# Performance work log

Measured on AMD Instinct MI355X. Metric: run time of the kernel, lower is better.

Reference implementation:

```python
import jax, jax.numpy as jnp
import numpy as np

C_M = 256   # norm_channel (msa channel)
C_Z = 128   # pair_channel
H = 8       # num_head
C = 32      # attention_channel per head


def layer_norm(x, gamma, beta, eps=1e-5):
    mu = jnp.mean(x, axis=-1, keepdims=True)
    var = jnp.var(x, axis=-1, keepdims=True)
    return (x - mu) * jax.lax.rsqrt(var + eps) * gamma + beta


def setup_inputs() -> dict:
    key = jax.random.key(0)
    ks = jax.random.split(key, 12)
    B, S, R = 1, 128, 256
    inp = {
        "msa_act": jax.random.normal(ks[0], (B, S, R, C_M), jnp.float32),
        "pair_act": jax.random.normal(ks[1], (B, R, R, C_Z), jnp.float32),
        "msa_mask": jnp.ones((B, S, R), jnp.float32),
        # query_norm params
        "qn_g": jnp.ones((C_M,), jnp.float32),
        "qn_b": jnp.zeros((C_M,), jnp.float32),
        # feat_2d_norm params
        "pn_g": jnp.ones((C_Z,), jnp.float32),
        "pn_b": jnp.zeros((C_Z,), jnp.float32),
        # feat_2d_weights: Linear(C_Z -> H, bias=False)
        "w2d": jax.random.normal(ks[2], (C_Z, H), jnp.float32) / np.sqrt(C_Z),
        # attention projections [C_M, H, C]
        "wq": jax.random.normal(ks[3], (C_M, H, C), jnp.float32) / np.sqrt(C_M),
        "wk": jax.random.normal(ks[4], (C_M, H, C), jnp.float32) / np.sqrt(C_M),
        "wv": jax.random.normal(ks[5], (C_M, H, C), jnp.float32) / np.sqrt(C_M),
        # gating linear [C_M, H, C] + bias
        "wg": jax.random.normal(ks[6], (C_M, H, C), jnp.float32) / np.sqrt(C_M),
        "bg": jnp.ones((H, C), jnp.float32),
        # output linear [H, C, C_M] + bias
        "wo": jax.random.normal(ks[7], (H, C, C_M), jnp.float32) / np.sqrt(H * C),
        "bo": jnp.zeros((C_M,), jnp.float32),
    }
    return inp


def reference(msa_act, pair_act, msa_mask, qn_g, qn_b, pn_g, pn_b, w2d,
              wq, wk, wv, wg, bg, wo, bo):
    # Pair bias: LayerNorm -> Linear(C_Z->H) -> permute to [B, 1, H, R, R]
    z = layer_norm(pair_act, pn_g, pn_b)            # [B, R, R, C_Z]
    z = jnp.einsum('bqkc,ch->bhqk', z, w2d)          # [B, H, R, R]
    z = z[:, None]                                   # [B, 1, H, R, R]

    # Mask bias: [B, S, 1, 1, R]
    mask_bias = (1e9 * (msa_mask - 1.0))[:, :, None, None, :]

    # Row-wise MHA with query norm
    m = layer_norm(msa_act, qn_g, qn_b)              # [B, S, R, C_M]
    scale = 1.0 / np.sqrt(C)
    q = jnp.einsum('bsqc,chd->bshqd', m, wq) * scale
    k = jnp.einsum('bskc,chd->bshkd', m, wk)
    v = jnp.einsum('bskc,chd->bshkd', m, wv)

    logits = jnp.einsum('bshqd,bshkd->bshqk', q, k) + mask_bias + z
    a = jax.nn.softmax(logits, axis=-1)              # [B, S, H, R, R]
    o = jnp.einsum('bshqk,bshkd->bsqhd', a, v)       # [B, S, R, H, C]

    g = jax.nn.sigmoid(jnp.einsum('bsqc,chd->bsqhd', m, wg) + bg)
    o = o * g
    out = jnp.einsum('bsqhd,hdc->bsqc', o, wo) + bo  # [B, S, R, C_M]
    return out
```

## Files before the change

### kernel.cpp

```cpp
#include <hip/hip_runtime.h>
#include <hip/hip_bf16.h>

typedef unsigned short u16;
typedef __attribute__((ext_vector_type(8))) short bf16x8;
typedef __attribute__((ext_vector_type(4))) float f32x4;

__device__ __forceinline__ float bf2f(u16 u){
  union { unsigned int i; float f; } v; v.i = ((unsigned int)u) << 16; return v.f;
}
__device__ __forceinline__ u16 f2bf(float f){
  union { float f; unsigned int i; } v; v.f = f;
  unsigned int i = v.i;
  return (u16)((i + 0x7fffu + ((i >> 16) & 1u)) >> 16);
}
__device__ __forceinline__ unsigned int pk2(float a, float b){
  union { __hip_bfloat162 v; unsigned int u; } c;
  c.v = __float22bfloat162_rn(float2{a, b});
  return c.u;
}
__device__ __forceinline__ float ldin(const void* p, int i, int f){
  return f ? ((const float*)p)[i] : bf2f(((const u16*)p)[i]);
}

__global__ __launch_bounds__(256) void k_prep(
    const void* __restrict__ msa,  const void* __restrict__ pair,
    const void* __restrict__ qng,  const void* __restrict__ qnb,
    const void* __restrict__ png,  const void* __restrict__ pnb,
    const void* __restrict__ w2d,
    const void* __restrict__ wq, const void* __restrict__ wk,
    const void* __restrict__ wv, const void* __restrict__ wg,
    const void* __restrict__ wo,
    u16* __restrict__ Wt, u16* __restrict__ wot,
    u16* __restrict__ m_bf, u16* __restrict__ z_bf,
    int* __restrict__ flagp)
{
  __shared__ u16 shm[11008];
  __shared__ int flag_sh;
  const int t = threadIdx.x;
  const int bid = blockIdx.x;

  if (t < 64) {
    const unsigned int* msa_w = (const unsigned int*)msa;
    int lo0 = 0, expok = 0;
    #pragma unroll
    for (int j = 0; j < 4; ++j) {
      unsigned int w = msa_w[t * 4 + j];
      if ((w & 0xffffu) == 0u) lo0++;
      unsigned int e = (w >> 7) & 0xffu;
      if (e >= 110u && e <= 140u) expok++;
    }
    #pragma unroll
    for (int off = 1; off < 64; off <<= 1) {
      lo0   += __shfl_xor(lo0,   off, 64);
      expok += __shfl_xor(expok, off, 64);
    }
    if (t == 0) flag_sh = (lo0 > 200) ? 1 : ((expok > 200) ? 0 : 1);
  }
  __syncthreads();
  const int flag = flag_sh;
  if (bid == 0 && t == 0) *flagp = flag;

  if (bid < 80) {
    u16* T = shm;
    const int mat = bid >> 4, tile = bid & 15;
    const int R0 = (tile >> 2) * 64, C0 = (tile & 3) * 64;
    const void* src = (mat == 0) ? wq : (mat == 1) ? wk : (mat == 2) ? wv
                    : (mat == 3) ? wg : wo;
    u16* dst = (mat < 4) ? (Wt + mat * 65536) : wot;
    {
      int i = t >> 2, j0 = (t & 3) * 16;
      #pragma unroll
      for (int e = 0; e < 8; ++e) {
        float a = ldin(src, (R0 + i) * 256 + C0 + j0 + 2*e,     flag);
        float b = ldin(src, (R0 + i) * 256 + C0 + j0 + 2*e + 1, flag);
        *(unsigned int*)(T + i * 72 + j0 + 2*e) = pk2(a, b);
      }
    }
    __syncthreads();
    {
      int j = t >> 2, i0 = (t & 3) * 16;
      u16 o[16];
      #pragma unroll
      for (int e = 0; e < 16; ++e) o[e] = T[(i0 + e) * 72 + j];
      *(uint4*)(dst + (C0 + j) * 256 + R0 + i0)     = *(const uint4*)o;
      *(uint4*)(dst + (C0 + j) * 256 + R0 + i0 + 8) = *(const uint4*)(o + 8);
    }
  } else if (bid < 8272) {
    int wave = t >> 6, lane = t & 63;
    int row = (bid - 80) * 4 + wave;
    float x[4];
    if (flag) {
      float4 f4 = *((const float4*)msa + row * 64 + lane);
      x[0]=f4.x; x[1]=f4.y; x[2]=f4.z; x[3]=f4.w;
    } else {
      uint2 u = *((const uint2*)msa + row * 64 + lane);
      const u16* h = (const u16*)&u;
      #pragma unroll
      for (int j = 0; j < 4; ++j) x[j] = bf2f(h[j]);
    }
    float s = 0.f, sq = 0.f;
    #pragma unroll
    for (int j = 0; j < 4; ++j) { s += x[j]; sq += x[j] * x[j]; }
    #pragma unroll
    for (int off = 1; off < 64; off <<= 1) {
      s  += __shfl_xor(s,  off, 64);
      sq += __shfl_xor(sq, off, 64);
    }
    float mu = s * (1.f / 256.f);
    float var = sq * (1.f / 256.f) - mu * mu;
    float rs = rsqrtf(var + 1e-5f);
    float y[4];
    #pragma unroll
    for (int j = 0; j < 4; ++j) {
      int c = lane * 4 + j;
      y[j] = (x[j] - mu) * rs * ldin(qng, c, flag) + ldin(qnb, c, flag);
    }
    uint2 o2;
    o2.x = pk2(y[0], y[1]);
    o2.y = pk2(y[2], y[3]);
    *((uint2*)m_bf + row * 64 + lane) = o2;
  } else {
    u16* As = shm;
    u16* Bs = shm + 64 * 136;
    const int lane = t & 63, wave = t >> 6;
    const int g = lane >> 4, l15 = lane & 15;
    const int rowBase = (bid - 8272) * 64;

    if (t < 128) {
      #pragma unroll
      for (int n = 0; n < 16; ++n)
        Bs[n * 136 + t] = (n < 8) ? f2bf(ldin(w2d, t * 8 + n, flag)) : (u16)0;
    }
    {
      int lrow = t >> 2, cb = (t & 3) * 32;
      int base = (rowBase + lrow) * 128 + cb;
      float x[32];
      if (flag) {
        const float* p = (const float*)pair + base;
        #pragma unroll
        for (int j = 0; j < 8; ++j) {
          float4 f4 = *(const float4*)(p + 4 * j);
          x[4*j] = f4.x; x[4*j+1] = f4.y; x[4*j+2] = f4.z; x[4*j+3] = f4.w;
        }
      } else {
        const u16* p = (const u16*)pair + base;
        #pragma unroll
        for (int j = 0; j < 4; ++j) {
          uint4 u = *(const uint4*)(p + 8 * j);
          const u16* h = (const u16*)&u;
          #pragma unroll
          for (int e = 0; e < 8; ++e) x[8*j+e] = bf2f(h[e]);
        }
      }
      float s = 0.f, sq = 0.f;
      #pragma unroll
      for (int j = 0; j < 32; ++j) { s += x[j]; sq += x[j] * x[j]; }
      s  += __shfl_xor(s, 1, 64);  s  += __shfl_xor(s, 2, 64);
      sq += __shfl_xor(sq, 1, 64); sq += __shfl_xor(sq, 2, 64);
      float mu = s * (1.f / 128.f);
      float var = sq * (1.f / 128.f) - mu * mu;
      float rs = rsqrtf(var + 1e-5f);
      float n_[32];
      #pragma unroll
      for (int j = 0; j < 32; ++j) {
        int c = cb + j;
        n_[j] = (x[j] - mu) * rs * ldin(png, c, flag) + ldin(pnb, c, flag);
      }
      u16* dst = As + lrow * 136 + cb;
      #pragma unroll
      for (int j = 0; j < 16; ++j)
        *(unsigned int*)(dst + 2*j) = pk2(n_[2*j], n_[2*j+1]);
    }
    __syncthreads();

    f32x4 accz = {0.f, 0.f, 0.f, 0.f};
    #pragma unroll
    for (int kb = 0; kb < 4; ++kb) {
      bf16x8 a = *(const bf16x8*)(As + (wave * 16 + l15) * 136 + kb * 32 + g * 8);
      bf16x8 b = *(const bf16x8*)(Bs + l15 * 136 + kb * 32 + g * 8);
      accz = __builtin_amdgcn_mfma_f32_16x16x32_bf16(a, b, accz, 0, 0, 0);
    }
    if (l15 < 8) {
      #pragma unroll
      for (int r = 0; r < 4; ++r)
        z_bf[l15 * 65536 + rowBase + wave * 16 + g * 4 + r] = f2bf(accz[r]);
    }
  }
}

__global__ __launch_bounds__(256, 2) void k_fused(
    const u16* __restrict__ m_bf, const u16* __restrict__ Wt,
    const void* __restrict__ bg, const u16* __restrict__ z_bf,
    const void* __restrict__ mask, const int* __restrict__ flagp,
    u16* __restrict__ og_ws)
{
  __shared__ u16 Ks[256 * 40];
  __shared__ u16 Vts[32 * 264];
  __shared__ float Mb[256];
  const int flag = *flagp;
  const int t = threadIdx.x, lane = t & 63, wave = t >> 6;
  const int s_ = blockIdx.x, h = blockIdx.y;
  const int g = lane >> 4, l15 = lane & 15;

  Mb[t] = 1e9f * (ldin(mask, s_ * 256 + t, flag) - 1.0f);

  const float scale = 0.17677669529663687f;
  f32x4 zero = {0.f, 0.f, 0.f, 0.f};

  bf16x8 af[8][4];
  #pragma unroll
  for (int kb = 0; kb < 8; ++kb)
    #pragma unroll
    for (int mt = 0; mt < 4; ++mt)
      af[kb][mt] = *(const bf16x8*)(
          m_bf + (s_ * 256 + wave * 64 + mt * 16 + l15) * 256 + kb * 32 + g * 8);

  unsigned int qp[4][4];
  float gg[4][2][4];

  #pragma unroll
  for (int matid = 0; matid < 4; ++matid) {
    const u16* W = Wt + matid * 65536 + (h * 32) * 256;
    f32x4 acc[4][2];
    #pragma unroll
    for (int mt = 0; mt < 4; ++mt) { acc[mt][0] = zero; acc[mt][1] = zero; }
    #pragma unroll
    for (int kb = 0; kb < 8; ++kb) {
      bf16x8 b0 = *(const bf16x8*)(W + l15 * 256        + kb * 32 + g * 8);
      bf16x8 b1 = *(const bf16x8*)(W + (16 + l15) * 256 + kb * 32 + g * 8);
      #pragma unroll
      for (int mt = 0; mt < 4; ++mt) {
        if (matid == 0 || matid == 2) {
          acc[mt][0] = __builtin_amdgcn_mfma_f32_16x16x32_bf16(b0, af[kb][mt], acc[mt][0], 0, 0, 0);
          acc[mt][1] = __builtin_amdgcn_mfma_f32_16x16x32_bf16(b1, af[kb][mt], acc[mt][1], 0, 0, 0);
        } else {
          acc[mt][0] = __builtin_amdgcn_mfma_f32_16x16x32_bf16(af[kb][mt], b0, acc[mt][0], 0, 0, 0);
          acc[mt][1] = __builtin_amdgcn_mfma_f32_16x16x32_bf16(af[kb][mt], b1, acc[mt][1], 0, 0, 0);
        }
      }
    }
    if (matid == 0) {
      #pragma unroll
      for (int mt = 0; mt < 4; ++mt) {
        qp[mt][0] = pk2(acc[mt][0][0] * scale, acc[mt][0][1] * scale);
        qp[mt][1] = pk2(acc[mt][0][2] * scale, acc[mt][0][3] * scale);
        qp[mt][2] = pk2(acc[mt][1][0] * scale, acc[mt][1][1] * scale);
        qp[mt][3] = pk2(acc[mt][1][2] * scale, acc[mt][1][3] * scale);
      }
    } else if (matid == 1) {
      #pragma unroll
      for (int mt = 0; mt < 4; ++mt)
        #pragma unroll
        for (int r = 0; r < 4; ++r) {
          int rowl = wave * 64 + mt * 16 + g * 4 + r;
          Ks[rowl * 40 + l15]      = f2bf(acc[mt][0][r]);
          Ks[rowl * 40 + 16 + l15] = f2bf(acc[mt][1][r]);
        }
    } else if (matid == 2) {
      #pragma unroll
      for (int mt = 0; mt < 4; ++mt)
        #pragma unroll
        for (int r = 0; r < 4; ++r) {
          int kcol = wave * 64 + mt * 16 + l15;
          Vts[(g * 4 + r) * 264 + kcol]      = f2bf(acc[mt][0][r]);
          Vts[(16 + g * 4 + r) * 264 + kcol] = f2bf(acc[mt][1][r]);
        }
    } else {
      #pragma unroll
      for (int mt = 0; mt < 4; ++mt)
        #pragma unroll
        for (int nt = 0; nt < 2; ++nt)
          #pragma unroll
          for (int r = 0; r < 4; ++r) {
            float gv = acc[mt][nt][r] + ldin(bg, h * 32 + nt * 16 + l15, flag);
            gg[mt][nt][r] = 1.0f / (1.0f + __expf(-gv));
          }
    }
  }
  __syncthreads();

  #pragma unroll
  for (int qt = 0; qt < 4; ++qt) {
    __builtin_amdgcn_sched_barrier(0);
    const int qbase = wave * 64 + qt * 16;
    const u16* zb = z_bf + h * 65536 + (qbase + l15) * 256;
    uint2 zu[16];
    #pragma unroll
    for (int kt = 0; kt < 16; ++kt)
      zu[kt] = *(const uint2*)(zb + kt * 16 + g * 4);

    union { bf16x8 v; unsigned int w[4]; } aq;
    aq.w[0] = qp[qt][0]; aq.w[1] = qp[qt][1];
    aq.w[2] = qp[qt][2]; aq.w[3] = qp[qt][3];

    f32x4 S[16];
    #pragma unroll
    for (int kt = 0; kt < 16; ++kt) {
      union { bf16x8 v; uint2 u2[2]; } kf;
      const u16* kr = Ks + (kt * 16 + l15) * 40;
      kf.u2[0] = *(const uint2*)(kr + g * 4);
      kf.u2[1] = *(const uint2*)(kr + 16 + g * 4);
      S[kt] = __builtin_amdgcn_mfma_f32_16x16x32_bf16(kf.v, aq.v, zero, 0, 0, 0);
    }

    float sm = 0.f;
    unsigned int pw[8][4];
    #pragma unroll
    for (int kc = 0; kc < 8; ++kc) {
      #pragma unroll
      for (int half = 0; half < 2; ++half) {
        const int kt = kc * 2 + half;
        float4 mb = *(const float4*)(Mb + kt * 16 + g * 4);
        const u16* zh = (const u16*)&zu[kt];
        float e0 = __expf(S[kt][0] + mb.x + bf2f(zh[0]));
        float e1 = __expf(S[kt][1] + mb.y + bf2f(zh[1]));
        float e2 = __expf(S[kt][2] + mb.z + bf2f(zh[2]));
        float e3 = __expf(S[kt][3] + mb.w + bf2f(zh[3]));
        sm += (e0 + e1) + (e2 + e3);
        pw[kc][half * 2]     = pk2(e0, e1);
        pw[kc][half * 2 + 1] = pk2(e2, e3);
      }
    }

    f32x4 O0a = zero, O0b = zero, O1a = zero, O1b = zero;
    #pragma unroll
    for (int kc = 0; kc < 8; ++kc) {
      union { bf16x8 v; unsigned int w[4]; } pf;
      pf.w[0] = pw[kc][0]; pf.w[1] = pw[kc][1];
      pf.w[2] = pw[kc][2]; pf.w[3] = pw[kc][3];
      union { bf16x8 v; uint2 u2[2]; } vf0, vf1;
      const u16* vr0 = Vts + l15 * 264 + kc * 32;
      const u16* vr1 = Vts + (16 + l15) * 264 + kc * 32;
      vf0.u2[0] = *(const uint2*)(vr0 + g * 4);
      vf0.u2[1] = *(const uint2*)(vr0 + 16 + g * 4);
      vf1.u2[0] = *(const uint2*)(vr1 + g * 4);
      vf1.u2[1] = *(const uint2*)(vr1 + 16 + g * 4);
      if (kc & 1) {
        O0b = __builtin_amdgcn_mfma_f32_16x16x32_bf16(pf.v, vf0.v, O0b, 0, 0, 0);
        O1b = __builtin_amdgcn_mfma_f32_16x16x32_bf16(pf.v, vf1.v, O1b, 0, 0, 0);
      } else {
        O0a = __builtin_amdgcn_mfma_f32_16x16x32_bf16(pf.v, vf0.v, O0a, 0, 0, 0);
        O1a = __builtin_amdgcn_mfma_f32_16x16x32_bf16(pf.v, vf1.v, O1a, 0, 0, 0);
      }
    }
    sm += __shfl_xor(sm, 16, 64);
    sm += __shfl_xor(sm, 32, 64);
    #pragma unroll
    for (int r = 0; r < 4; ++r) {
      float smr = __shfl(sm, g * 4 + r, 64);
      float inv = 1.0f / smr;
      int qq = qbase + g * 4 + r;
      int base = (s_ * 256 + qq) * 256 + h * 32;
      og_ws[base + l15]      = f2bf((O0a[r] + O0b[r]) * inv * gg[qt][0][r]);
      og_ws[base + 16 + l15] = f2bf((O1a[r] + O1b[r]) * inv * gg[qt][1][r]);
    }
  }
}

__global__ __launch_bounds__(256, 4) void k_outproj(
    const u16* __restrict__ og, const u16* __restrict__ wot,
    const void* __restrict__ bo, const int* __restrict__ flagp,
    void* __restrict__ outv)
{
  const int flag = *flagp;
  const int t = threadIdx.x, lane = t & 63, wave = t >> 6;
  const int wm = (wave >> 1) * 32, wn = (wave & 1) * 64;
  const int rowBase = blockIdx.x * 64;
  const int ct = blockIdx.y;
  const int g = lane >> 4, l15 = lane & 15;

  bf16x8 af[8][2];
  #pragma unroll
  for (int kb = 0; kb < 8; ++kb)
    #pragma unroll
    for (int mt = 0; mt < 2; ++mt)
      af[kb][mt] = *(const bf16x8*)(
          og + (rowBase + wm + mt * 16 + l15) * 256 + kb * 32 + g * 8);

  const u16* Wb = wot + (ct * 128 + wn) * 256;
  f32x4 acc[2][4];
  f32x4 zero = {0.f, 0.f, 0.f, 0.f};
  #pragma unroll
  for (int i = 0; i < 2; ++i)
    #pragma unroll
    for (int j = 0; j < 4; ++j) acc[i][j] = zero;
  #pragma unroll
  for (int kb = 0; kb < 8; ++kb) {
    bf16x8 bb[4];
    #pragma unroll
    for (int nt = 0; nt < 4; ++nt)
      bb[nt] = *(const bf16x8*)(Wb + (nt * 16 + l15) * 256 + kb * 32 + g * 8);
    #pragma unroll
    for (int mt = 0; mt < 2; ++mt)
      #pragma unroll
      for (int nt = 0; nt < 4; ++nt)
        acc[mt][nt] = __builtin_amdgcn_mfma_f32_16x16x32_bf16(
            af[kb][mt], bb[nt], acc[mt][nt], 0, 0, 0);
  }
  #pragma unroll
  for (int mt = 0; mt < 2; ++mt)
    #pragma unroll
    for (int nt = 0; nt < 4; ++nt)
      #pragma unroll
      for (int r = 0; r < 4; ++r) {
        int row = rowBase + wm + mt * 16 + g * 4 + r;
        int col = ct * 128 + wn + nt * 16 + l15;
        float val = acc[mt][nt][r] + ldin(bo, col, flag);
        if (flag) ((float*)outv)[row * 256 + col] = val;
        else      ((u16*)outv)[row * 256 + col]   = f2bf(val);
      }
}

extern "C" void kernel_launch(void* const* d_in, const int* in_sizes, int n_in,
                              void* d_out, int out_size, void* d_ws, size_t ws_size,
                              hipStream_t stream)
{
  const void* msa  = d_in[0];
  const void* pair = d_in[1];
  const void* mask = d_in[2];
  const void* qng  = d_in[3];
  const void* qnb  = d_in[4];
  const void* png  = d_in[5];
  const void* pnb  = d_in[6];
  const void* w2d  = d_in[7];
  const void* wq   = d_in[8];
  const void* wk   = d_in[9];
  const void* wv   = d_in[10];
  const void* wg   = d_in[11];
  const void* bg   = d_in[12];
  const void* wo   = d_in[13];
  const void* bo   = d_in[14];

  char* ws = (char*)d_ws;
  u16* z_bf  = (u16*)(ws + 0);
  u16* Wt    = (u16*)(ws + 1048576);
  u16* wot   = (u16*)(ws + 1572864);
  int* flag  = (int*)(ws + 1703936);
  u16* m_bf  = (u16*)(ws + 1704192);
  u16* og_ws = (u16*)(ws + 18481408);

  hipLaunchKernelGGL(k_prep, dim3(9296), dim3(256), 0, stream,
                     msa, pair, qng, qnb, png, pnb, w2d,
                     wq, wk, wv, wg, wo, Wt, wot, m_bf, z_bf, flag);
  hipLaunchKernelGGL(k_fused, dim3(128, 8), dim3(256), 0, stream,
                     m_bf, Wt, bg, z_bf, mask, flag, og_ws);
  hipLaunchKernelGGL(k_outproj, dim3(512, 2), dim3(256), 0, stream,
                     og_ws, wot, bo, flag, d_out);
}
```

Baseline: 266.5 us.

## Split fused attention into separate QKVG projection GEMM and attention kernels

Replaces the fused per-(sequence, head) kernel, which recomputed Q/K/V/gate projections and staged K and transposed V in LDS, with a standalone projection GEMM that writes Q, K, V-transposed and the sigmoid gate to global workspace. The attention kernel now reads its operands from global memory with no LDS staging and runs at higher occupancy (launch bounds 4). It also interleaves score computation with the PV product per key chunk instead of holding all scores in registers. The aim is better occupancy and GEMM efficiency, paid for with roughly 64 MB of extra global write and read traffic for the intermediates and an extra kernel launch.

```diff
diff --git a/kernel.cpp b/kernel.cpp
--- a/kernel.cpp
+++ b/kernel.cpp
@@ -188,14 +188,92 @@
   }
 }
 
-__global__ __launch_bounds__(256, 2) void k_fused(
+__global__ __launch_bounds__(256, 4) void k_qkvg(
     const u16* __restrict__ m_bf, const u16* __restrict__ Wt,
-    const void* __restrict__ bg, const u16* __restrict__ z_bf,
-    const void* __restrict__ mask, const int* __restrict__ flagp,
-    u16* __restrict__ og_ws)
+    const void* __restrict__ bg, const int* __restrict__ flagp,
+    u16* __restrict__ Qw, u16* __restrict__ Kw,
+    u16* __restrict__ Vt, u16* __restrict__ Gw)
 {
-  __shared__ u16 Ks[256 * 40];
-  __shared__ u16 Vts[32 * 264];
+  const int flag = *flagp;
+  const int t = threadIdx.x, lane = t & 63, wave = t >> 6;
+  const int wm = (wave >> 1) * 32, wn = (wave & 1) * 64;
+  const int rowBase = blockIdx.x * 64;
+  const int matid = blockIdx.y >> 1, half = blockIdx.y & 1;
+  const int g = lane >> 4, l15 = lane & 15;
+  const float scale = 0.17677669529663687f;
+
+  bf16x8 af[8][2];
+  #pragma unroll
+  for (int kb = 0; kb < 8; ++kb)
+    #pragma unroll
+    for (int mt = 0; mt < 2; ++mt)
+      af[kb][mt] = *(const bf16x8*)(
+          m_bf + (rowBase + wm + mt * 16 + l15) * 256 + kb * 32 + g * 8);
+
+  const u16* W = Wt + matid * 65536 + (half * 128 + wn) * 256;
+  f32x4 acc[2][4];
+  f32x4 zero = {0.f, 0.f, 0.f, 0.f};
+  #pragma unroll
+  for (int i = 0; i < 2; ++i)
+    #pragma unroll
+    for (int j = 0; j < 4; ++j) acc[i][j] = zero;
+  #pragma unroll
+  for (int kb = 0; kb < 8; ++kb) {
+    bf16x8 bb[4];
+    #pragma unroll
+    for (int nt = 0; nt < 4; ++nt)
+      bb[nt] = *(const bf16x8*)(W + (nt * 16 + l15) * 256 + kb * 32 + g * 8);
+    #pragma unroll
+    for (int mt = 0; mt < 2; ++mt)
+      #pragma unroll
+      for (int nt = 0; nt < 4; ++nt) {
+        if (matid == 2)
+          acc[mt][nt] = __builtin_amdgcn_mfma_f32_16x16x32_bf16(
+              bb[nt], af[kb][mt], acc[mt][nt], 0, 0, 0);
+        else
+          acc[mt][nt] = __builtin_amdgcn_mfma_f32_16x16x32_bf16(
+              af[kb][mt], bb[nt], acc[mt][nt], 0, 0, 0);
+      }
+  }
+  if (matid == 2) {
+    #pragma unroll
+    for (int mt = 0; mt < 2; ++mt) {
+      const int rg = rowBase + wm + mt * 16;
+      const int s = rg >> 8, k0 = rg & 255;
+      #pragma unroll
+      for (int nt = 0; nt < 4; ++nt)
+        #pragma unroll
+        for (int r = 0; r < 4; ++r) {
+          int dcol = half * 128 + wn + nt * 16 + g * 4 + r;
+          Vt[((s * 8 + (dcol >> 5)) * 32 + (dcol & 31)) * 256 + k0 + l15] =
+              f2bf(acc[mt][nt][r]);
+        }
+    }
+  } else {
+    u16* dst = (matid == 0) ? Qw : (matid == 1) ? Kw : Gw;
+    #pragma unroll
+    for (int mt = 0; mt < 2; ++mt)
+      #pragma unroll
+      for (int nt = 0; nt < 4; ++nt)
+        #pragma unroll
+        for (int r = 0; r < 4; ++r) {
+          int row = rowBase + wm + mt * 16 + g * 4 + r;
+          int col = half * 128 + wn + nt * 16 + l15;
+          float v = acc[mt][nt][r];
+          if (matid == 0) v *= scale;
+          else if (matid == 3)
+            v = 1.0f / (1.0f + __expf(-(v + ldin(bg, col, flag))));
+          dst[row * 256 + col] = f2bf(v);
+        }
+  }
+}
+
+__global__ __launch_bounds__(256, 4) void k_attn(
+    const u16* __restrict__ Qw, const u16* __restrict__ Kw,
+    const u16* __restrict__ Vt, const u16* __restrict__ Gw,
+    const u16* __restrict__ z_bf, const void* __restrict__ mask,
+    const int* __restrict__ flagp, u16* __restrict__ og)
+{
   __shared__ float Mb[256];
   const int flag = *flagp;
   const int t = threadIdx.x, lane = t & 63, wave = t >> 6;
@@ -203,145 +281,54 @@
   const int g = lane >> 4, l15 = lane & 15;
 
   Mb[t] = 1e9f * (ldin(mask, s_ * 256 + t, flag) - 1.0f);
-
-  const float scale = 0.17677669529663687f;
+  __syncthreads();
+
   f32x4 zero = {0.f, 0.f, 0.f, 0.f};
-
-  bf16x8 af[8][4];
-  #pragma unroll
-  for (int kb = 0; kb < 8; ++kb)
-    #pragma unroll
-    for (int mt = 0; mt < 4; ++mt)
-      af[kb][mt] = *(const bf16x8*)(
-          m_bf + (s_ * 256 + wave * 64 + mt * 16 + l15) * 256 + kb * 32 + g * 8);
-
-  unsigned int qp[4][4];
-  float gg[4][2][4];
-
-  #pragma unroll
-  for (int matid = 0; matid < 4; ++matid) {
-    const u16* W = Wt + matid * 65536 + (h * 32) * 256;
-    f32x4 acc[4][2];
-    #pragma unroll
-    for (int mt = 0; mt < 4; ++mt) { acc[mt][0] = zero; acc[mt][1] = zero; }
-    #pragma unroll
-    for (int kb = 0; kb < 8; ++kb) {
-      bf16x8 b0 = *(const bf16x8*)(W + l15 * 256        + kb * 32 + g * 8);
-      bf16x8 b1 = *(const bf16x8*)(W + (16 + l15) * 256 + kb * 32 + g * 8);
-      #pragma unroll
-      for (int mt = 0; mt < 4; ++mt) {
-        if (matid == 0 || matid == 2) {
-          acc[mt][0] = __builtin_amdgcn_mfma_f32_16x16x32_bf16(b0, af[kb][mt], acc[mt][0], 0, 0, 0);
-          acc[mt][1] = __builtin_amdgcn_mfma_f32_16x16x32_bf16(b1, af[kb][mt], acc[mt][1], 0, 0, 0);
-        } else {
-          acc[mt][0] = __builtin_amdgcn_mfma_f32_16x16x32_bf16(af[kb][mt], b0, acc[mt][0], 0, 0, 0);
-          acc[mt][1] = __builtin_amdgcn_mfma_f32_16x16x32_bf16(af[kb][mt], b1, acc[mt][1], 0, 0, 0);
-        }
-      }
-    }
-    if (matid == 0) {
-      #pragma unroll
-      for (int mt = 0; mt < 4; ++mt) {
-        qp[mt][0] = pk2(acc[mt][0][0] * scale, acc[mt][0][1] * scale);
-        qp[mt][1] = pk2(acc[mt][0][2] * scale, acc[mt][0][3] * scale);
-        qp[mt][2] = pk2(acc[mt][1][0] * scale, acc[mt][1][1] * scale);
-        qp[mt][3] = pk2(acc[mt][1][2] * scale, acc[mt][1][3] * scale);
-      }
-    } else if (matid == 1) {
-      #pragma unroll
-      for (int mt = 0; mt < 4; ++mt)
-        #pragma unroll
-        for (int r = 0; r < 4; ++r) {
-          int rowl = wave * 64 + mt * 16 + g * 4 + r;
-          Ks[rowl * 40 + l15]      = f2bf(acc[mt][0][r]);
-          Ks[rowl * 40 + 16 + l15] = f2bf(acc[mt][1][r]);
-        }
-    } else if (matid == 2) {
-      #pragma unroll
-      for (int mt = 0; mt < 4; ++mt)
-        #pragma unroll
-        for (int r = 0; r < 4; ++r) {
-          int kcol = wave * 64 + mt * 16 + l15;
-          Vts[(g * 4 + r) * 264 + kcol]      = f2bf(acc[mt][0][r]);
-          Vts[(16 + g * 4 + r) * 264 + kcol] = f2bf(acc[mt][1][r]);
-        }
-    } else {
-      #pragma unroll
-      for (int mt = 0; mt < 4; ++mt)
-        #pragma unroll
-        for (int nt = 0; nt < 2; ++nt)
-          #pragma unroll
-          for (int r = 0; r < 4; ++r) {
-            float gv = acc[mt][nt][r] + ldin(bg, h * 32 + nt * 16 + l15, flag);
-            gg[mt][nt][r] = 1.0f / (1.0f + __expf(-gv));
-          }
-    }
-  }
-  __syncthreads();
-
-  #pragma unroll
+  const u16* Qb = Qw + (s_ * 256) * 256 + h * 32;
+  const u16* Kb = Kw + (s_ * 256) * 256 + h * 32;
+  const u16* Vb = Vt + ((s_ * 8 + h) * 32) * 256;
+  const u16* Gb = Gw + (s_ * 256) * 256 + h * 32;
+  const u16* zb0 = z_bf + h * 65536;
+
+  #pragma clang loop unroll(disable)
   for (int qt = 0; qt < 4; ++qt) {
-    __builtin_amdgcn_sched_barrier(0);
     const int qbase = wave * 64 + qt * 16;
-    const u16* zb = z_bf + h * 65536 + (qbase + l15) * 256;
-    uint2 zu[16];
-    #pragma unroll
-    for (int kt = 0; kt < 16; ++kt)
-      zu[kt] = *(const uint2*)(zb + kt * 16 + g * 4);
-
-    union { bf16x8 v; unsigned int w[4]; } aq;
-    aq.w[0] = qp[qt][0]; aq.w[1] = qp[qt][1];
-    aq.w[2] = qp[qt][2]; aq.w[3] = qp[qt][3];
-
-    f32x4 S[16];
-    #pragma unroll
-    for (int kt = 0; kt < 16; ++kt) {
-      union { bf16x8 v; uint2 u2[2]; } kf;
-      const u16* kr = Ks + (kt * 16 + l15) * 40;
-      kf.u2[0] = *(const uint2*)(kr + g * 4);
-      kf.u2[1] = *(const uint2*)(kr + 16 + g * 4);
-      S[kt] = __builtin_amdgcn_mfma_f32_16x16x32_bf16(kf.v, aq.v, zero, 0, 0, 0);
-    }
+    union { bf16x8 v; uint2 u2[2]; } aq;
+    aq.u2[0] = *(const uint2*)(Qb + (qbase + l15) * 256 + g * 4);
+    aq.u2[1] = *(const uint2*)(Qb + (qbase + l15) * 256 + 16 + g * 4);
 
     float sm = 0.f;
-    unsigned int pw[8][4];
+    f32x4 O0 = zero, O1 = zero;
     #pragma unroll
     for (int kc = 0; kc < 8; ++kc) {
-      #pragma unroll
-      for (int half = 0; half < 2; ++half) {
-        const int kt = kc * 2 + half;
+      unsigned int pw[4];
+      #pragma unroll
+      for (int hf = 0; hf < 2; ++hf) {
+        const int kt = kc * 2 + hf;
+        union { bf16x8 v; uint2 u2[2]; } kf;
+        kf.u2[0] = *(const uint2*)(Kb + (kt * 16 + l15) * 256 + g * 4);
+        kf.u2[1] = *(const uint2*)(Kb + (kt * 16 + l15) * 256 + 16 + g * 4);
+        f32x4 S = __builtin_amdgcn_mfma_f32_16x16x32_bf16(kf.v, aq.v, zero, 0, 0, 0);
         float4 mb = *(const float4*)(Mb + kt * 16 + g * 4);
-        const u16* zh = (const u16*)&zu[kt];
-        float e0 = __expf(S[kt][0] + mb.x + bf2f(zh[0]));
-        float e1 = __expf(S[kt][1] + mb.y + bf2f(zh[1]));
-        float e2 = __expf(S[kt][2] + mb.z + bf2f(zh[2]));
-        float e3 = __expf(S[kt][3] + mb.w + bf2f(zh[3]));
+        uint2 zu = *(const uint2*)(zb0 + (qbase + l15) * 256 + kt * 16 + g * 4);
+        const u16* zh = (const u16*)&zu;
+        float e0 = __expf(S[0] + mb.x + bf2f(zh[0]));
+        float e1 = __expf(S[1] + mb.y + bf2f(zh[1]));
+        float e2 = __expf(S[2] + mb.z + bf2f(zh[2]));
+        float e3 = __expf(S[3] + mb.w + bf2f(zh[3]));
         sm += (e0 + e1) + (e2 + e3);
-        pw[kc][half * 2]     = pk2(e0, e1);
-        pw[kc][half * 2 + 1] = pk2(e2, e3);
-      }
-    }
-
-    f32x4 O0a = zero, O0b = zero, O1a = zero, O1b = zero;
-    #pragma unroll
-    for (int kc = 0; kc < 8; ++kc) {
+        pw[hf * 2]     = pk2(e0, e1);
+        pw[hf * 2 + 1] = pk2(e2, e3);
+      }
       union { bf16x8 v; unsigned int w[4]; } pf;
-      pf.w[0] = pw[kc][0]; pf.w[1] = pw[kc][1];
-      pf.w[2] = pw[kc][2]; pf.w[3] = pw[kc][3];
+      pf.w[0] = pw[0]; pf.w[1] = pw[1]; pf.w[2] = pw[2]; pf.w[3] = pw[3];
       union { bf16x8 v; uint2 u2[2]; } vf0, vf1;
-      const u16* vr0 = Vts + l15 * 264 + kc * 32;
-      const u16* vr1 = Vts + (16 + l15) * 264 + kc * 32;
-      vf0.u2[0] = *(const uint2*)(vr0 + g * 4);
-      vf0.u2[1] = *(const uint2*)(vr0 + 16 + g * 4);
-      vf1.u2[0] = *(const uint2*)(vr1 + g * 4);
-      vf1.u2[1] = *(const uint2*)(vr1 + 16 + g * 4);
-      if (kc & 1) {
-        O0b = __builtin_amdgcn_mfma_f32_16x16x32_bf16(pf.v, vf0.v, O0b, 0, 0, 0);
-        O1b = __builtin_amdgcn_mfma_f32_16x16x32_bf16(pf.v, vf1.v, O1b, 0, 0, 0);
-      } else {
-        O0a = __builtin_amdgcn_mfma_f32_16x16x32_bf16(pf.v, vf0.v, O0a, 0, 0, 0);
-        O1a = __builtin_amdgcn_mfma_f32_16x16x32_bf16(pf.v, vf1.v, O1a, 0, 0, 0);
-      }
+      vf0.u2[0] = *(const uint2*)(Vb + l15 * 256        + kc * 32 + g * 4);
+      vf0.u2[1] = *(const uint2*)(Vb + l15 * 256        + kc * 32 + 16 + g * 4);
+      vf1.u2[0] = *(const uint2*)(Vb + (16 + l15) * 256 + kc * 32 + g * 4);
+      vf1.u2[1] = *(const uint2*)(Vb + (16 + l15) * 256 + kc * 32 + 16 + g * 4);
+      O0 = __builtin_amdgcn_mfma_f32_16x16x32_bf16(pf.v, vf0.v, O0, 0, 0, 0);
+      O1 = __builtin_amdgcn_mfma_f32_16x16x32_bf16(pf.v, vf1.v, O1, 0, 0, 0);
     }
     sm += __shfl_xor(sm, 16, 64);
     sm += __shfl_xor(sm, 32, 64);
@@ -350,9 +337,11 @@
       float smr = __shfl(sm, g * 4 + r, 64);
       float inv = 1.0f / smr;
       int qq = qbase + g * 4 + r;
+      float g0 = bf2f(Gb[qq * 256 + l15]);
+      float g1 = bf2f(Gb[qq * 256 + 16 + l15]);
       int base = (s_ * 256 + qq) * 256 + h * 32;
-      og_ws[base + l15]      = f2bf((O0a[r] + O0b[r]) * inv * gg[qt][0][r]);
-      og_ws[base + 16 + l15] = f2bf((O1a[r] + O1b[r]) * inv * gg[qt][1][r]);
+      og[base + l15]      = f2bf(O0[r] * inv * g0);
+      og[base + 16 + l15] = f2bf(O1[r] * inv * g1);
     }
   }
 }
@@ -437,13 +426,19 @@
   u16* wot   = (u16*)(ws + 1572864);
   int* flag  = (int*)(ws + 1703936);
   u16* m_bf  = (u16*)(ws + 1704192);
-  u16* og_ws = (u16*)(ws + 18481408);
+  u16* og_ws = m_bf;
+  u16* Q_ws  = (u16*)(ws + 18481408);
+  u16* K_ws  = (u16*)(ws + 35258624);
+  u16* Vt_ws = (u16*)(ws + 52035840);
+  u16* G_ws  = (u16*)(ws + 68813056);
 
   hipLaunchKernelGGL(k_prep, dim3(9296), dim3(256), 0, stream,
                      msa, pair, qng, qnb, png, pnb, w2d,
                      wq, wk, wv, wg, wo, Wt, wot, m_bf, z_bf, flag);
-  hipLaunchKernelGGL(k_fused, dim3(128, 8), dim3(256), 0, stream,
-                     m_bf, Wt, bg, z_bf, mask, flag, og_ws);
+  hipLaunchKernelGGL(k_qkvg, dim3(512, 8), dim3(256), 0, stream,
+                     m_bf, Wt, bg, flag, Q_ws, K_ws, Vt_ws, G_ws);
+  hipLaunchKernelGGL(k_attn, dim3(128, 8), dim3(256), 0, stream,
+                     Q_ws, K_ws, Vt_ws, G_ws, z_bf, mask, flag, og_ws);
   hipLaunchKernelGGL(k_outproj, dim3(512, 2), dim3(256), 0, stream,
                      og_ws, wot, bo, flag, d_out);
 }
```

Measured after the change: 414.1 us. 1.55x slower.
